# Performance work log

Measured on AMD Instinct MI355X. Metric: run time of the kernel, lower is better.

## Reference

```python
import jax, jax.numpy as jnp
import numpy as np

N, E, P = 50000, 500000, 10000
F_IN, H, C = 128, 256, 1


def gat_conv(x, src, dst, W, a_s, a_d, b):
    # single-head GATConv (PyG): h = x W; e_ij = LeakyReLU(a_s.h_j + a_d.h_i)
    n = x.shape[0]
    h = x @ W                              # [n, out]
    es = h @ a_s                           # [n]
    ed = h @ a_d                           # [n]
    logits = jax.nn.leaky_relu(es[src] + ed[dst], 0.2)   # [E']
    m = jax.ops.segment_max(logits, dst, num_segments=n)
    p = jnp.exp(logits - m[dst])
    denom = jax.ops.segment_sum(p, dst, num_segments=n)
    alpha = p / denom[dst]                 # edge-softmax over incoming edges
    out = jax.ops.segment_sum(h[src] * alpha[:, None], dst, num_segments=n)
    return out + b


def setup_inputs():
    key = jax.random.key(0)
    ks = jax.random.split(key, 14)
    inp = {
        "features": jax.random.normal(ks[0], (N, F_IN), jnp.float32),
        "edge_index": jax.random.randint(ks[1], (2, E), 0, N, dtype=jnp.int32),
        "mask": jax.random.randint(ks[2], (P, 2), 0, N, dtype=jnp.int32),
        "W1": jax.random.normal(ks[3], (F_IN, H), jnp.float32) / np.sqrt(F_IN),
        "a_src1": jax.random.normal(ks[4], (H,), jnp.float32) / np.sqrt(H),
        "a_dst1": jax.random.normal(ks[5], (H,), jnp.float32) / np.sqrt(H),
        "b1": jnp.zeros((H,), jnp.float32),
        "W2": jax.random.normal(ks[6], (H, F_IN), jnp.float32) / np.sqrt(H),
        "a_src2": jax.random.normal(ks[7], (F_IN,), jnp.float32) / np.sqrt(F_IN),
        "a_dst2": jax.random.normal(ks[8], (F_IN,), jnp.float32) / np.sqrt(F_IN),
        "b2": jnp.zeros((F_IN,), jnp.float32),
        "Wl": jax.random.normal(ks[9], (2 * F_IN, C), jnp.float32) / np.sqrt(2 * F_IN),
        "bl": jnp.zeros((C,), jnp.float32),
    }
    return inp


def reference(features, edge_index, mask, W1, a_src1, a_dst1, b1, W2, a_src2, a_dst2, b2, Wl, bl):
    n = features.shape[0]
    loop = jnp.arange(n, dtype=edge_index.dtype)   # PyG add_self_loops=True
    src = jnp.concatenate([edge_index[0], loop])
    dst = jnp.concatenate([edge_index[1], loop])
    h = gat_conv(features, src, dst, W1, a_src1, a_dst1, b1)   # [N, H]
    h = jax.nn.relu(h)                                         # dropout=0.0
    h = gat_conv(h, src, dst, W2, a_src2, a_dst2, b2)          # [N, F_IN]
    mT = mask.T
    p1 = jax.lax.stop_gradient(h[mT[0]])   # .detach() in original
    p2 = jax.lax.stop_gradient(h[mT[1]])
    z = jnp.concatenate([p1, p2], axis=1)  # [P, 2*F_IN]
    return jax.nn.sigmoid(z @ Wl + bl)
```

## Files before the change

### kernel.cpp

```cpp
#include <hip/hip_runtime.h>
#include <hip/hip_bf16.h>
#include <math.h>

#define NN 50000
#define NE 500000
#define NP 10000
#define FIN 128
#define HD 256
#define CAP 64
#define NBG 391

typedef __attribute__((ext_vector_type(8))) short bf16x8;
typedef __attribute__((ext_vector_type(4))) float f32x4;
typedef __attribute__((ext_vector_type(2))) float f32x2;

__device__ inline unsigned short f2bf(float f) {
  unsigned int u = __float_as_uint(f);
  unsigned int r = (u + 0x7fffu + ((u >> 16) & 1u)) >> 16;
  return (unsigned short)r;
}

__device__ inline unsigned int cvtpk_bf16(float lo, float hi) {
  unsigned int r;
  asm("v_cvt_pk_bf16_f32 %0, %1, %2" : "=v"(r) : "v"(lo), "v"(hi));
  return r;
}

__device__ inline float bflo(unsigned int u) { return __uint_as_float(u << 16); }
__device__ inline float bfhi(unsigned int u) { return __uint_as_float(u & 0xffff0000u); }

__device__ inline unsigned char f2fp8(float v) {
  int pk = __builtin_amdgcn_cvt_pk_fp8_f32(v, v, 0, false);
  return (unsigned char)(pk & 0xff);
}

__global__ void init_prep(int* __restrict__ deg,
                          const float* __restrict__ W1, const float* __restrict__ W2,
                          unsigned short* __restrict__ W1T, unsigned short* __restrict__ W2T) {
  int idx = blockIdx.x * 256 + threadIdx.x;
  if (idx < NN) deg[idx] = 0;
  if (idx < FIN * HD) {
    int n = idx / FIN, k = idx - n * FIN;
    W1T[idx] = f2bf(W1[(size_t)k * HD + n]);
    int n2 = idx / HD, k2 = idx - n2 * HD;
    W2T[idx] = f2bf(W2[(size_t)k2 * FIN + n2]);
  }
}

template <int BN, int KTOT, bool A_BF16, bool C_FP8>
__global__ __launch_bounds__(512)
void gemm_hist(const void* __restrict__ Aptr, const unsigned short* __restrict__ BT,
               void* __restrict__ Cptr, const float* __restrict__ a_s,
               const float* __restrict__ a_d, float* __restrict__ es, float* __restrict__ ed,
               int M, const int* __restrict__ dst, int* __restrict__ deg,
               int* __restrict__ rank) {
  if (blockIdx.x >= NBG) {
    int e = (blockIdx.x - NBG) * 512 + threadIdx.x;
    if (e < NE) rank[e] = atomicAdd(&deg[dst[e]], 1);
    return;
  }
  constexpr int LDK = 72;
  constexpr int CN = BN / 2;
  constexpr int NT = CN / 16;
  __shared__ unsigned short As[128][LDK];
  __shared__ unsigned short Bs[BN][LDK];
  __shared__ float esl[128][2];
  __shared__ float edl[128][2];
  const int tid = threadIdx.x;
  const int wave = tid >> 6;
  const int lane = tid & 63;
  const int quad = lane >> 4;
  const int l16 = lane & 15;
  const int wrow = wave >> 1;
  const int wcol = wave & 1;
  const int row0 = blockIdx.x * 128;

  f32x4 acc[2][NT] = {};

  for (int k0 = 0; k0 < KTOT; k0 += 64) {
#pragma unroll
    for (int p = 0; p < 4; p++) {
      int m = p * 32 + (tid >> 4);
      int k4 = (tid & 15) * 4;
      int gr = row0 + m;
      uint2 pk = make_uint2(0u, 0u);
      if (gr < M) {
        if (A_BF16) {
          pk = *(const uint2*)((const unsigned short*)Aptr + (size_t)gr * KTOT + k0 + k4);
        } else {
          float4 v = *(const float4*)((const float*)Aptr + (size_t)gr * KTOT + k0 + k4);
          pk.x = cvtpk_bf16(v.x, v.y);
          pk.y = cvtpk_bf16(v.z, v.w);
        }
      }
      *(uint2*)&As[m][k4] = pk;
    }
#pragma unroll
    for (int p = 0; p < BN / 64; p++) {
      int n = p * 64 + (tid >> 3);
      int k8 = (tid & 7) * 8;
      *(uint4*)&Bs[n][k8] = *(const uint4*)(BT + (size_t)n * KTOT + k0 + k8);
    }
    __syncthreads();
#pragma unroll
    for (int ks = 0; ks < 2; ks++) {
      bf16x8 afrag[2];
#pragma unroll
      for (int rt = 0; rt < 2; rt++)
        afrag[rt] = *(const bf16x8*)&As[wrow * 32 + rt * 16 + l16][ks * 32 + quad * 8];
#pragma unroll
      for (int ct = 0; ct < NT; ct++) {
        bf16x8 bfrag = *(const bf16x8*)&Bs[wcol * CN + ct * 16 + l16][ks * 32 + quad * 8];
#pragma unroll
        for (int rt = 0; rt < 2; rt++)
          acc[rt][ct] = __builtin_amdgcn_mfma_f32_16x16x32_bf16(afrag[rt], bfrag, acc[rt][ct], 0, 0, 0);
      }
    }
    __syncthreads();
  }

  float asv[NT], adv[NT];
#pragma unroll
  for (int ct = 0; ct < NT; ct++) {
    asv[ct] = a_s[wcol * CN + ct * 16 + l16];
    adv[ct] = a_d[wcol * CN + ct * 16 + l16];
  }
#pragma unroll
  for (int rt = 0; rt < 2; rt++) {
#pragma unroll
    for (int r = 0; r < 4; r++) {
      int lrow = wrow * 32 + rt * 16 + quad * 4 + r;
      int grow = row0 + lrow;
      bool ok = (grow < M);
      float ps = 0.f, pd = 0.f;
#pragma unroll
      for (int ct = 0; ct < NT; ct++) {
        float v = acc[rt][ct][r];
        ps += v * asv[ct];
        pd += v * adv[ct];
        if (ok) {
          size_t cidx = (size_t)grow * BN + wcol * CN + ct * 16 + l16;
          if (C_FP8) ((unsigned char*)Cptr)[cidx] = f2fp8(v);
          else       ((unsigned short*)Cptr)[cidx] = f2bf(v);
        }
      }
#pragma unroll
      for (int off = 1; off < 16; off <<= 1) {
        ps += __shfl_xor(ps, off, 16);
        pd += __shfl_xor(pd, off, 16);
      }
      if (l16 == 0) {
        esl[lrow][wcol] = ps;
        edl[lrow][wcol] = pd;
      }
    }
  }
  __syncthreads();
  if (tid < 128) {
    int grow = row0 + tid;
    if (grow < M) {
      es[grow] = esl[tid][0] + esl[tid][1];
      ed[grow] = edl[tid][0] + edl[tid][1];
    }
  }
}

__global__ void scatter_kernel(const int* __restrict__ src, const int* __restrict__ dst,
                               const int* __restrict__ rank, const int* __restrict__ deg,
                               int* __restrict__ ssrc) {
  int t = blockIdx.x * blockDim.x + threadIdx.x;
  int e = t * 2;
  if (e < NE) {
    int2 d2 = *(const int2*)(dst + e);
    int2 s2 = *(const int2*)(src + e);
    int2 r2 = *(const int2*)(rank + e);
    if (r2.x < CAP - 1) ssrc[d2.x * CAP + r2.x] = s2.x;
    if (r2.y < CAP - 1) ssrc[d2.y * CAP + r2.y] = s2.y;
  } else {
    int i = t - NE / 2;
    if (i < NN) ssrc[i * CAP + min(deg[i], CAP - 1)] = i;
  }
}

template <int BN, int KTOT, bool A_BF16, bool C_FP8>
__global__ __launch_bounds__(512)
void mfma_gemm(const void* __restrict__ Aptr, const unsigned short* __restrict__ BT,
               void* __restrict__ Cptr, const float* __restrict__ a_s,
               const float* __restrict__ a_d, float* __restrict__ es, float* __restrict__ ed,
               int M) {
  constexpr int LDK = 72;
  constexpr int CN = BN / 2;
  constexpr int NT = CN / 16;
  __shared__ unsigned short As[128][LDK];
  __shared__ unsigned short Bs[BN][LDK];
  __shared__ float esl[128][2];
  __shared__ float edl[128][2];
  const int tid = threadIdx.x;
  const int wave = tid >> 6;
  const int lane = tid & 63;
  const int quad = lane >> 4;
  const int l16 = lane & 15;
  const int wrow = wave >> 1;
  const int wcol = wave & 1;
  const int row0 = blockIdx.x * 128;

  f32x4 acc[2][NT] = {};

  for (int k0 = 0; k0 < KTOT; k0 += 64) {
#pragma unroll
    for (int p = 0; p < 4; p++) {
      int m = p * 32 + (tid >> 4);
      int k4 = (tid & 15) * 4;
      int gr = row0 + m;
      uint2 pk = make_uint2(0u, 0u);
      if (gr < M) {
        if (A_BF16) {
          pk = *(const uint2*)((const unsigned short*)Aptr + (size_t)gr * KTOT + k0 + k4);
        } else {
          float4 v = *(const float4*)((const float*)Aptr + (size_t)gr * KTOT + k0 + k4);
          pk.x = cvtpk_bf16(v.x, v.y);
          pk.y = cvtpk_bf16(v.z, v.w);
        }
      }
      *(uint2*)&As[m][k4] = pk;
    }
#pragma unroll
    for (int p = 0; p < BN / 64; p++) {
      int n = p * 64 + (tid >> 3);
      int k8 = (tid & 7) * 8;
      *(uint4*)&Bs[n][k8] = *(const uint4*)(BT + (size_t)n * KTOT + k0 + k8);
    }
    __syncthreads();
#pragma unroll
    for (int ks = 0; ks < 2; ks++) {
      bf16x8 afrag[2];
#pragma unroll
      for (int rt = 0; rt < 2; rt++)
        afrag[rt] = *(const bf16x8*)&As[wrow * 32 + rt * 16 + l16][ks * 32 + quad * 8];
#pragma unroll
      for (int ct = 0; ct < NT; ct++) {
        bf16x8 bfrag = *(const bf16x8*)&Bs[wcol * CN + ct * 16 + l16][ks * 32 + quad * 8];
#pragma unroll
        for (int rt = 0; rt < 2; rt++)
          acc[rt][ct] = __builtin_amdgcn_mfma_f32_16x16x32_bf16(afrag[rt], bfrag, acc[rt][ct], 0, 0, 0);
      }
    }
    __syncthreads();
  }

  float asv[NT], adv[NT];
#pragma unroll
  for (int ct = 0; ct < NT; ct++) {
    asv[ct] = a_s[wcol * CN + ct * 16 + l16];
    adv[ct] = a_d[wcol * CN + ct * 16 + l16];
  }
#pragma unroll
  for (int rt = 0; rt < 2; rt++) {
#pragma unroll
    for (int r = 0; r < 4; r++) {
      int lrow = wrow * 32 + rt * 16 + quad * 4 + r;
      int grow = row0 + lrow;
      bool ok = (grow < M);
      float ps = 0.f, pd = 0.f;
#pragma unroll
      for (int ct = 0; ct < NT; ct++) {
        float v = acc[rt][ct][r];
        ps += v * asv[ct];
        pd += v * adv[ct];
        if (ok) {
          size_t cidx = (size_t)grow * BN + wcol * CN + ct * 16 + l16;
          if (C_FP8) ((unsigned char*)Cptr)[cidx] = f2fp8(v);
          else       ((unsigned short*)Cptr)[cidx] = f2bf(v);
        }
      }
#pragma unroll
      for (int off = 1; off < 16; off <<= 1) {
        ps += __shfl_xor(ps, off, 16);
        pd += __shfl_xor(pd, off, 16);
      }
      if (l16 == 0) {
        esl[lrow][wcol] = ps;
        edl[lrow][wcol] = pd;
      }
    }
  }
  __syncthreads();
  if (tid < 128) {
    int grow = row0 + tid;
    if (grow < M) {
      es[grow] = esl[tid][0] + esl[tid][1];
      ed[grow] = edl[tid][0] + edl[tid][1];
    }
  }
}

__global__ __launch_bounds__(256)
void fused_agg64(const int* __restrict__ deg, const int* __restrict__ ssrc,
                 const float* __restrict__ es, const float* __restrict__ ed,
                 const unsigned char* __restrict__ h, const float* __restrict__ bias,
                 unsigned short* __restrict__ outp, int n) {
  int i = blockIdx.x * 16 + (threadIdx.x >> 4);
  int ls = threadIdx.x & 15;
  if (i >= n) return;
  int s = i * CAP;
  int e = s + min(deg[i] + 1, CAP);
  float edv = ed[i];

  float acc[16] = {};
  float lsum = 0.f;
  const unsigned char* hb = h + ls * 16;
  for (int p0 = s; p0 < e; p0 += 16) {
    int p = p0 + ls;
    int msrc = 0;
    float pv = 0.f;
    if (p < e) {
      msrc = ssrc[p];
      float t = es[msrc] + edv;
      float lg = (t > 0.f) ? t : 0.2f * t;
      pv = __expf(lg);
    }
    lsum += pv;
    int cnt = min(16, e - p0);
    int jfull = cnt & ~3;
    for (int j = 0; j < jfull; j += 4) {
      uint4 r[4];
      float w[4];
#pragma unroll
      for (int u = 0; u < 4; u++) {
        int jj = j + u;
        int sj = __shfl(msrc, jj, 16);
        w[u] = __shfl(pv, jj, 16);
        r[u] = *(const uint4*)(hb + (size_t)sj * HD);
      }
#pragma unroll
      for (int u = 0; u < 4; u++) {
        f32x2 lo, hi;
        lo = __builtin_amdgcn_cvt_pk_f32_fp8(r[u].x, false);
        hi = __builtin_amdgcn_cvt_pk_f32_fp8(r[u].x, true);
        acc[0] += w[u] * lo.x; acc[1] += w[u] * lo.y; acc[2] += w[u] * hi.x; acc[3] += w[u] * hi.y;
        lo = __builtin_amdgcn_cvt_pk_f32_fp8(r[u].y, false);
        hi = __builtin_amdgcn_cvt_pk_f32_fp8(r[u].y, true);
        acc[4] += w[u] * lo.x; acc[5] += w[u] * lo.y; acc[6] += w[u] * hi.x; acc[7] += w[u] * hi.y;
        lo = __builtin_amdgcn_cvt_pk_f32_fp8(r[u].z, false);
        hi = __builtin_amdgcn_cvt_pk_f32_fp8(r[u].z, true);
        acc[8] += w[u] * lo.x; acc[9] += w[u] * lo.y; acc[10] += w[u] * hi.x; acc[11] += w[u] * hi.y;
        lo = __builtin_amdgcn_cvt_pk_f32_fp8(r[u].w, false);
        hi = __builtin_amdgcn_cvt_pk_f32_fp8(r[u].w, true);
        acc[12] += w[u] * lo.x; acc[13] += w[u] * lo.y; acc[14] += w[u] * hi.x; acc[15] += w[u] * hi.y;
      }
    }
    if (jfull < cnt) {
      uint4 r[4];
      float w[4];
#pragma unroll
      for (int u = 0; u < 4; u++) {
        int jj = jfull + u;
        bool ok = jj < cnt;
        int jc = ok ? jj : 0;
        int sj = __shfl(msrc, jc, 16);
        float wr = __shfl(pv, jc, 16);
        w[u] = ok ? wr : 0.f;
        r[u] = *(const uint4*)(hb + (size_t)sj * HD);
      }
#pragma unroll
      for (int u = 0; u < 4; u++) {
        f32x2 lo, hi;
        lo = __builtin_amdgcn_cvt_pk_f32_fp8(r[u].x, false);
        hi = __builtin_amdgcn_cvt_pk_f32_fp8(r[u].x, true);
        acc[0] += w[u] * lo.x; acc[1] += w[u] * lo.y; acc[2] += w[u] * hi.x; acc[3] += w[u] * hi.y;
        lo = __builtin_amdgcn_cvt_pk_f32_fp8(r[u].y, false);
        hi = __builtin_amdgcn_cvt_pk_f32_fp8(r[u].y, true);
        acc[4] += w[u] * lo.x; acc[5] += w[u] * lo.y; acc[6] += w[u] * hi.x; acc[7] += w[u] * hi.y;
        lo = __builtin_amdgcn_cvt_pk_f32_fp8(r[u].z, false);
        hi = __builtin_amdgcn_cvt_pk_f32_fp8(r[u].z, true);
        acc[8] += w[u] * lo.x; acc[9] += w[u] * lo.y; acc[10] += w[u] * hi.x; acc[11] += w[u] * hi.y;
        lo = __builtin_amdgcn_cvt_pk_f32_fp8(r[u].w, false);
        hi = __builtin_amdgcn_cvt_pk_f32_fp8(r[u].w, true);
        acc[12] += w[u] * lo.x; acc[13] += w[u] * lo.y; acc[14] += w[u] * hi.x; acc[15] += w[u] * hi.y;
      }
    }
  }
#pragma unroll
  for (int off = 8; off; off >>= 1) lsum += __shfl_xor(lsum, off, 16);
  float invd = 1.0f / lsum;
  float4 b0 = *(const float4*)(bias + ls * 16 + 0);
  float4 b1 = *(const float4*)(bias + ls * 16 + 4);
  float4 b2 = *(const float4*)(bias + ls * 16 + 8);
  float4 b3 = *(const float4*)(bias + ls * 16 + 12);
  float v0 = fmaxf(acc[0] * invd + b0.x, 0.f),  v1 = fmaxf(acc[1] * invd + b0.y, 0.f);
  float v2 = fmaxf(acc[2] * invd + b0.z, 0.f),  v3 = fmaxf(acc[3] * invd + b0.w, 0.f);
  float v4 = fmaxf(acc[4] * invd + b1.x, 0.f),  v5 = fmaxf(acc[5] * invd + b1.y, 0.f);
  float v6 = fmaxf(acc[6] * invd + b1.z, 0.f),  v7 = fmaxf(acc[7] * invd + b1.w, 0.f);
  float v8 = fmaxf(acc[8] * invd + b2.x, 0.f),  v9 = fmaxf(acc[9] * invd + b2.y, 0.f);
  float va = fmaxf(acc[10] * invd + b2.z, 0.f), vb = fmaxf(acc[11] * invd + b2.w, 0.f);
  float vc = fmaxf(acc[12] * invd + b3.x, 0.f), vd = fmaxf(acc[13] * invd + b3.y, 0.f);
  float ve = fmaxf(acc[14] * invd + b3.z, 0.f), vf = fmaxf(acc[15] * invd + b3.w, 0.f);
  unsigned short* ob = outp + (size_t)i * HD + ls * 16;
  *(uint4*)(ob) = make_uint4(cvtpk_bf16(v0, v1), cvtpk_bf16(v2, v3),
                             cvtpk_bf16(v4, v5), cvtpk_bf16(v6, v7));
  *(uint4*)(ob + 8) = make_uint4(cvtpk_bf16(v8, v9), cvtpk_bf16(va, vb),
                                 cvtpk_bf16(vc, vd), cvtpk_bf16(ve, vf));
}

__global__ __launch_bounds__(256)
void fused_agg_l2_pair(const int* __restrict__ deg, const int* __restrict__ ssrc,
                       const float* __restrict__ es, const float* __restrict__ ed,
                       const unsigned short* __restrict__ h, const float* __restrict__ bias,
                       const int* __restrict__ mask, const float* __restrict__ Wl,
                       const float* __restrict__ bl, float* __restrict__ out, int P) {
  constexpr int F = FIN;
  int pair = blockIdx.x * 8 + (threadIdx.x >> 5);
  if (pair >= P) return;
  int l32 = threadIdx.x & 31;
  int hf = l32 >> 4;
  int ls = l32 & 15;
  int i = mask[pair * 2 + hf];
  int s = i * CAP;
  int e = s + min(deg[i] + 1, CAP);
  float edv = ed[i];

  float acc[8] = {};
  float lsum = 0.f;
  const unsigned short* hb = h + ls * 8;
  for (int p0 = s; p0 < e; p0 += 16) {
    int p = p0 + ls;
    int msrc = 0;
    float pv = 0.f;
    if (p < e) {
      msrc = ssrc[p];
      float t = es[msrc] + edv;
      float lg = (t > 0.f) ? t : 0.2f * t;
      pv = __expf(lg);
    }
    lsum += pv;
    int cnt = min(16, e - p0);
    int jfull = cnt & ~3;
    for (int j = 0; j < jfull; j += 4) {
      uint4 r[4];
      float w[4];
#pragma unroll
      for (int u = 0; u < 4; u++) {
        int jj = j + u;
        int sj = __shfl(msrc, jj, 16);
        w[u] = __shfl(pv, jj, 16);
        r[u] = *(const uint4*)(hb + (size_t)sj * F);
      }
#pragma unroll
      for (int u = 0; u < 4; u++) {
        acc[0] += w[u] * bflo(r[u].x); acc[1] += w[u] * bfhi(r[u].x);
        acc[2] += w[u] * bflo(r[u].y); acc[3] += w[u] * bfhi(r[u].y);
        acc[4] += w[u] * bflo(r[u].z); acc[5] += w[u] * bfhi(r[u].z);
        acc[6] += w[u] * bflo(r[u].w); acc[7] += w[u] * bfhi(r[u].w);
      }
    }
    if (jfull < cnt) {
      uint4 r[4];
      float w[4];
#pragma unroll
      for (int u = 0; u < 4; u++) {
        int jj = jfull + u;
        bool ok = jj < cnt;
        int jc = ok ? jj : 0;
        int sj = __shfl(msrc, jc, 16);
        float wr = __shfl(pv, jc, 16);
        w[u] = ok ? wr : 0.f;
        r[u] = *(const uint4*)(hb + (size_t)sj * F);
      }
#pragma unroll
      for (int u = 0; u < 4; u++) {
        acc[0] += w[u] * bflo(r[u].x); acc[1] += w[u] * bfhi(r[u].x);
        acc[2] += w[u] * bflo(r[u].y); acc[3] += w[u] * bfhi(r[u].y);
        acc[4] += w[u] * bflo(r[u].z); acc[5] += w[u] * bfhi(r[u].z);
        acc[6] += w[u] * bflo(r[u].w); acc[7] += w[u] * bfhi(r[u].w);
      }
    }
  }
#pragma unroll
  for (int off = 8; off; off >>= 1) lsum += __shfl_xor(lsum, off, 16);
  float invd = 1.0f / lsum;
  float4 b0 = *(const float4*)(bias + ls * 8 + 0);
  float4 b1 = *(const float4*)(bias + ls * 8 + 4);
  float4 w0 = *(const float4*)(Wl + hf * F + ls * 8 + 0);
  float4 w1 = *(const float4*)(Wl + hf * F + ls * 8 + 4);
  float dotv = (acc[0] * invd + b0.x) * w0.x + (acc[1] * invd + b0.y) * w0.y +
               (acc[2] * invd + b0.z) * w0.z + (acc[3] * invd + b0.w) * w0.w +
               (acc[4] * invd + b1.x) * w1.x + (acc[5] * invd + b1.y) * w1.y +
               (acc[6] * invd + b1.z) * w1.z + (acc[7] * invd + b1.w) * w1.w;
#pragma unroll
  for (int off = 8; off; off >>= 1) dotv += __shfl_xor(dotv, off, 16);
  float othr = __shfl_xor(dotv, 16, 32);
  if (l32 == 0) {
    float z = dotv + othr + bl[0];
    out[pair] = 1.0f / (1.0f + expf(-z));
  }
}

extern "C" void kernel_launch(void* const* d_in, const int* in_sizes, int n_in,
                              void* d_out, int out_size, void* d_ws, size_t ws_size,
                              hipStream_t stream) {
  const float* features = (const float*)d_in[0];
  const int* edge_index = (const int*)d_in[1];
  const int* mask       = (const int*)d_in[2];
  const float* W1     = (const float*)d_in[3];
  const float* a_src1 = (const float*)d_in[4];
  const float* a_dst1 = (const float*)d_in[5];
  const float* b1     = (const float*)d_in[6];
  const float* W2     = (const float*)d_in[7];
  const float* a_src2 = (const float*)d_in[8];
  const float* a_dst2 = (const float*)d_in[9];
  const float* b2     = (const float*)d_in[10];
  const float* Wl     = (const float*)d_in[11];
  const float* bl     = (const float*)d_in[12];
  float* out = (float*)d_out;

  const int* src = edge_index;
  const int* dst = edge_index + NE;

  char* ws = (char*)d_ws;
  size_t off = 0;
  auto alloc = [&](size_t bytes) {
    void* p = ws + off;
    off += (bytes + 255) & ~(size_t)255;
    return p;
  };
  unsigned char* h1q = (unsigned char*)alloc((size_t)NN * HD);
  unsigned short* h2b = (unsigned short*)alloc((size_t)NN * FIN * 2);
  unsigned short* x2b = (unsigned short*)alloc((size_t)NN * HD * 2);
  unsigned short* W1T = (unsigned short*)alloc((size_t)HD * FIN * 2);
  unsigned short* W2T = (unsigned short*)alloc((size_t)FIN * HD * 2);
  float* es_buf  = (float*)alloc((size_t)NN * 4);
  float* ed_buf  = (float*)alloc((size_t)NN * 4);
  int* deg       = (int*)alloc((size_t)NN * 4);
  int* rank      = (int*)alloc((size_t)NE * 4);
  int* ssrc      = (int*)alloc((size_t)NN * CAP * 4);
  (void)ws_size; (void)in_sizes; (void)n_in; (void)out_size;

  const int nblk_n256 = (NN + 255) / 256;
  const int nblk_hist = (NE + 511) / 512;
  const int nblk_scat = (NE / 2 + NN + 255) / 256;

  init_prep<<<nblk_n256, 256, 0, stream>>>(deg, W1, W2, W1T, W2T);
  gemm_hist<HD, FIN, false, true><<<NBG + nblk_hist, 512, 0, stream>>>(
      (const void*)features, W1T, (void*)h1q, a_src1, a_dst1, es_buf, ed_buf, NN,
      dst, deg, rank);
  scatter_kernel<<<nblk_scat, 256, 0, stream>>>(src, dst, rank, deg, ssrc);
  fused_agg64<<<(NN + 15) / 16, 256, 0, stream>>>(
      deg, ssrc, es_buf, ed_buf, h1q, b1, x2b, NN);
  mfma_gemm<FIN, HD, true, false><<<(NN + 127) / 128, 512, 0, stream>>>(
      (const void*)x2b, W2T, (void*)h2b, a_src2, a_dst2, es_buf, ed_buf, NN);
  fused_agg_l2_pair<<<(NP + 7) / 8, 256, 0, stream>>>(
      deg, ssrc, es_buf, ed_buf, h2b, b2, mask, Wl, bl, out, NP);
}
```

Measured before the change: 188.8 us.

## Project layer-2 features onto classifier weights before aggregation

Because the final classifier is linear, the layer-2 GEMM now computes per-node scalar projections h2·Wl[0:128] and h2·Wl[128:256] instead of writing the full bf16 h2 matrix. The pair-prediction kernel then aggregates these scalars with the attention weights rather than gathering 128-wide rows. This removes the h2 write and the wide gather traffic, at the cost of a slightly different floating-point summation order.

```diff
diff --git a/kernel.cpp b/kernel.cpp
--- a/kernel.cpp
+++ b/kernel.cpp
@@ -47,10 +47,10 @@
   }
 }
 
-template <int BN, int KTOT, bool A_BF16, bool C_FP8>
+template <int BN, int KTOT>
 __global__ __launch_bounds__(512)
-void gemm_hist(const void* __restrict__ Aptr, const unsigned short* __restrict__ BT,
-               void* __restrict__ Cptr, const float* __restrict__ a_s,
+void gemm_hist(const float* __restrict__ Aptr, const unsigned short* __restrict__ BT,
+               unsigned char* __restrict__ Cptr, const float* __restrict__ a_s,
                const float* __restrict__ a_d, float* __restrict__ es, float* __restrict__ ed,
                int M, const int* __restrict__ dst, int* __restrict__ deg,
                int* __restrict__ rank) {
@@ -85,13 +85,9 @@
       int gr = row0 + m;
       uint2 pk = make_uint2(0u, 0u);
       if (gr < M) {
-        if (A_BF16) {
-          pk = *(const uint2*)((const unsigned short*)Aptr + (size_t)gr * KTOT + k0 + k4);
-        } else {
-          float4 v = *(const float4*)((const float*)Aptr + (size_t)gr * KTOT + k0 + k4);
-          pk.x = cvtpk_bf16(v.x, v.y);
-          pk.y = cvtpk_bf16(v.z, v.w);
-        }
+        float4 v = *(const float4*)(Aptr + (size_t)gr * KTOT + k0 + k4);
+        pk.x = cvtpk_bf16(v.x, v.y);
+        pk.y = cvtpk_bf16(v.z, v.w);
       }
       *(uint2*)&As[m][k4] = pk;
     }
@@ -140,8 +136,7 @@
         pd += v * adv[ct];
         if (ok) {
           size_t cidx = (size_t)grow * BN + wcol * CN + ct * 16 + l16;
-          if (C_FP8) ((unsigned char*)Cptr)[cidx] = f2fp8(v);
-          else       ((unsigned short*)Cptr)[cidx] = f2bf(v);
+          Cptr[cidx] = f2fp8(v);
         }
       }
 #pragma unroll
@@ -182,12 +177,13 @@
   }
 }
 
-template <int BN, int KTOT, bool A_BF16, bool C_FP8>
+template <int BN, int KTOT>
 __global__ __launch_bounds__(512)
-void mfma_gemm(const void* __restrict__ Aptr, const unsigned short* __restrict__ BT,
-               void* __restrict__ Cptr, const float* __restrict__ a_s,
-               const float* __restrict__ a_d, float* __restrict__ es, float* __restrict__ ed,
-               int M) {
+void gemm2_dots(const unsigned short* __restrict__ Aptr, const unsigned short* __restrict__ BT,
+                const float* __restrict__ a_s, const float* __restrict__ a_d,
+                const float* __restrict__ wl0, const float* __restrict__ wl1,
+                float* __restrict__ es, float* __restrict__ ed,
+                float* __restrict__ g0, float* __restrict__ g1, int M) {
   constexpr int LDK = 72;
   constexpr int CN = BN / 2;
   constexpr int NT = CN / 16;
@@ -195,6 +191,8 @@
   __shared__ unsigned short Bs[BN][LDK];
   __shared__ float esl[128][2];
   __shared__ float edl[128][2];
+  __shared__ float g0l[128][2];
+  __shared__ float g1l[128][2];
   const int tid = threadIdx.x;
   const int wave = tid >> 6;
   const int lane = tid & 63;
@@ -213,15 +211,8 @@
       int k4 = (tid & 15) * 4;
       int gr = row0 + m;
       uint2 pk = make_uint2(0u, 0u);
-      if (gr < M) {
-        if (A_BF16) {
-          pk = *(const uint2*)((const unsigned short*)Aptr + (size_t)gr * KTOT + k0 + k4);
-        } else {
-          float4 v = *(const float4*)((const float*)Aptr + (size_t)gr * KTOT + k0 + k4);
-          pk.x = cvtpk_bf16(v.x, v.y);
-          pk.y = cvtpk_bf16(v.z, v.w);
-        }
-      }
+      if (gr < M)
+        pk = *(const uint2*)(Aptr + (size_t)gr * KTOT + k0 + k4);
       *(uint2*)&As[m][k4] = pk;
     }
 #pragma unroll
@@ -248,39 +239,41 @@
     __syncthreads();
   }
 
-  float asv[NT], adv[NT];
+  float asv[NT], adv[NT], w0v[NT], w1v[NT];
 #pragma unroll
   for (int ct = 0; ct < NT; ct++) {
-    asv[ct] = a_s[wcol * CN + ct * 16 + l16];
-    adv[ct] = a_d[wcol * CN + ct * 16 + l16];
+    int col = wcol * CN + ct * 16 + l16;
+    asv[ct] = a_s[col];
+    adv[ct] = a_d[col];
+    w0v[ct] = wl0[col];
+    w1v[ct] = wl1[col];
   }
 #pragma unroll
   for (int rt = 0; rt < 2; rt++) {
 #pragma unroll
     for (int r = 0; r < 4; r++) {
       int lrow = wrow * 32 + rt * 16 + quad * 4 + r;
-      int grow = row0 + lrow;
-      bool ok = (grow < M);
-      float ps = 0.f, pd = 0.f;
+      float ps = 0.f, pd = 0.f, p0 = 0.f, p1 = 0.f;
 #pragma unroll
       for (int ct = 0; ct < NT; ct++) {
         float v = acc[rt][ct][r];
         ps += v * asv[ct];
         pd += v * adv[ct];
-        if (ok) {
-          size_t cidx = (size_t)grow * BN + wcol * CN + ct * 16 + l16;
-          if (C_FP8) ((unsigned char*)Cptr)[cidx] = f2fp8(v);
-          else       ((unsigned short*)Cptr)[cidx] = f2bf(v);
-        }
+        p0 += v * w0v[ct];
+        p1 += v * w1v[ct];
       }
 #pragma unroll
       for (int off = 1; off < 16; off <<= 1) {
         ps += __shfl_xor(ps, off, 16);
         pd += __shfl_xor(pd, off, 16);
+        p0 += __shfl_xor(p0, off, 16);
+        p1 += __shfl_xor(p1, off, 16);
       }
       if (l16 == 0) {
         esl[lrow][wcol] = ps;
         edl[lrow][wcol] = pd;
+        g0l[lrow][wcol] = p0;
+        g1l[lrow][wcol] = p1;
       }
     }
   }
@@ -290,6 +283,8 @@
     if (grow < M) {
       es[grow] = esl[tid][0] + esl[tid][1];
       ed[grow] = edl[tid][0] + edl[tid][1];
+      g0[grow] = g0l[tid][0] + g0l[tid][1];
+      g1[grow] = g1l[tid][0] + g1l[tid][1];
     }
   }
 }
@@ -403,12 +398,12 @@
 }
 
 __global__ __launch_bounds__(256)
-void fused_agg_l2_pair(const int* __restrict__ deg, const int* __restrict__ ssrc,
-                       const float* __restrict__ es, const float* __restrict__ ed,
-                       const unsigned short* __restrict__ h, const float* __restrict__ bias,
-                       const int* __restrict__ mask, const float* __restrict__ Wl,
-                       const float* __restrict__ bl, float* __restrict__ out, int P) {
-  constexpr int F = FIN;
+void predict_l2(const int* __restrict__ deg, const int* __restrict__ ssrc,
+                const float* __restrict__ es, const float* __restrict__ ed,
+                const float* __restrict__ g0, const float* __restrict__ g1,
+                const float* __restrict__ b2, const int* __restrict__ mask,
+                const float* __restrict__ Wl, const float* __restrict__ bl,
+                float* __restrict__ out, int P) {
   int pair = blockIdx.x * 8 + (threadIdx.x >> 5);
   if (pair >= P) return;
   int l32 = threadIdx.x & 31;
@@ -416,81 +411,34 @@
   int ls = l32 & 15;
   int i = mask[pair * 2 + hf];
   int s = i * CAP;
-  int e = s + min(deg[i] + 1, CAP);
+  int cnt = min(deg[i] + 1, CAP);
   float edv = ed[i];
-
-  float acc[8] = {};
-  float lsum = 0.f;
-  const unsigned short* hb = h + ls * 8;
-  for (int p0 = s; p0 < e; p0 += 16) {
-    int p = p0 + ls;
-    int msrc = 0;
-    float pv = 0.f;
-    if (p < e) {
-      msrc = ssrc[p];
-      float t = es[msrc] + edv;
-      float lg = (t > 0.f) ? t : 0.2f * t;
-      pv = __expf(lg);
-    }
+  const float* g = hf ? g1 : g0;
+
+  float lsum = 0.f, accg = 0.f;
+  for (int k = ls; k < cnt; k += 16) {
+    int m = ssrc[s + k];
+    float t = es[m] + edv;
+    float lg = (t > 0.f) ? t : 0.2f * t;
+    float pv = __expf(lg);
     lsum += pv;
-    int cnt = min(16, e - p0);
-    int jfull = cnt & ~3;
-    for (int j = 0; j < jfull; j += 4) {
-      uint4 r[4];
-      float w[4];
-#pragma unroll
-      for (int u = 0; u < 4; u++) {
-        int jj = j + u;
-        int sj = __shfl(msrc, jj, 16);
-        w[u] = __shfl(pv, jj, 16);
-        r[u] = *(const uint4*)(hb + (size_t)sj * F);
-      }
-#pragma unroll
-      for (int u = 0; u < 4; u++) {
-        acc[0] += w[u] * bflo(r[u].x); acc[1] += w[u] * bfhi(r[u].x);
-        acc[2] += w[u] * bflo(r[u].y); acc[3] += w[u] * bfhi(r[u].y);
-        acc[4] += w[u] * bflo(r[u].z); acc[5] += w[u] * bfhi(r[u].z);
-        acc[6] += w[u] * bflo(r[u].w); acc[7] += w[u] * bfhi(r[u].w);
-      }
-    }
-    if (jfull < cnt) {
-      uint4 r[4];
-      float w[4];
-#pragma unroll
-      for (int u = 0; u < 4; u++) {
-        int jj = jfull + u;
-        bool ok = jj < cnt;
-        int jc = ok ? jj : 0;
-        int sj = __shfl(msrc, jc, 16);
-        float wr = __shfl(pv, jc, 16);
-        w[u] = ok ? wr : 0.f;
-        r[u] = *(const uint4*)(hb + (size_t)sj * F);
-      }
-#pragma unroll
-      for (int u = 0; u < 4; u++) {
-        acc[0] += w[u] * bflo(r[u].x); acc[1] += w[u] * bfhi(r[u].x);
-        acc[2] += w[u] * bflo(r[u].y); acc[3] += w[u] * bfhi(r[u].y);
-        acc[4] += w[u] * bflo(r[u].z); acc[5] += w[u] * bfhi(r[u].z);
-        acc[6] += w[u] * bflo(r[u].w); acc[7] += w[u] * bfhi(r[u].w);
-      }
-    }
-  }
-#pragma unroll
-  for (int off = 8; off; off >>= 1) lsum += __shfl_xor(lsum, off, 16);
-  float invd = 1.0f / lsum;
-  float4 b0 = *(const float4*)(bias + ls * 8 + 0);
-  float4 b1 = *(const float4*)(bias + ls * 8 + 4);
-  float4 w0 = *(const float4*)(Wl + hf * F + ls * 8 + 0);
-  float4 w1 = *(const float4*)(Wl + hf * F + ls * 8 + 4);
-  float dotv = (acc[0] * invd + b0.x) * w0.x + (acc[1] * invd + b0.y) * w0.y +
-               (acc[2] * invd + b0.z) * w0.z + (acc[3] * invd + b0.w) * w0.w +
-               (acc[4] * invd + b1.x) * w1.x + (acc[5] * invd + b1.y) * w1.y +
-               (acc[6] * invd + b1.z) * w1.z + (acc[7] * invd + b1.w) * w1.w;
-#pragma unroll
-  for (int off = 8; off; off >>= 1) dotv += __shfl_xor(dotv, off, 16);
-  float othr = __shfl_xor(dotv, 16, 32);
+    accg += pv * g[m];
+  }
+  float accb = 0.f;
+  const float* wv = Wl + hf * FIN + ls * 8;
+  const float* bv = b2 + ls * 8;
+#pragma unroll
+  for (int q = 0; q < 8; q++) accb += bv[q] * wv[q];
+#pragma unroll
+  for (int off = 8; off; off >>= 1) {
+    lsum += __shfl_xor(lsum, off, 16);
+    accg += __shfl_xor(accg, off, 16);
+    accb += __shfl_xor(accb, off, 16);
+  }
+  float zs = accg / lsum + accb;
+  float othr = __shfl_xor(zs, 16, 32);
   if (l32 == 0) {
-    float z = dotv + othr + bl[0];
+    float z = zs + othr + bl[0];
     out[pair] = 1.0f / (1.0f + expf(-z));
   }
 }
@@ -524,12 +472,13 @@
     return p;
   };
   unsigned char* h1q = (unsigned char*)alloc((size_t)NN * HD);
-  unsigned short* h2b = (unsigned short*)alloc((size_t)NN * FIN * 2);
   unsigned short* x2b = (unsigned short*)alloc((size_t)NN * HD * 2);
   unsigned short* W1T = (unsigned short*)alloc((size_t)HD * FIN * 2);
   unsigned short* W2T = (unsigned short*)alloc((size_t)FIN * HD * 2);
   float* es_buf  = (float*)alloc((size_t)NN * 4);
   float* ed_buf  = (float*)alloc((size_t)NN * 4);
+  float* g0_buf  = (float*)alloc((size_t)NN * 4);
+  float* g1_buf  = (float*)alloc((size_t)NN * 4);
   int* deg       = (int*)alloc((size_t)NN * 4);
   int* rank      = (int*)alloc((size_t)NE * 4);
   int* ssrc      = (int*)alloc((size_t)NN * CAP * 4);
@@ -540,14 +489,13 @@
   const int nblk_scat = (NE / 2 + NN + 255) / 256;
 
   init_prep<<<nblk_n256, 256, 0, stream>>>(deg, W1, W2, W1T, W2T);
-  gemm_hist<HD, FIN, false, true><<<NBG + nblk_hist, 512, 0, stream>>>(
-      (const void*)features, W1T, (void*)h1q, a_src1, a_dst1, es_buf, ed_buf, NN,
-      dst, deg, rank);
+  gemm_hist<HD, FIN><<<NBG + nblk_hist, 512, 0, stream>>>(
+      features, W1T, h1q, a_src1, a_dst1, es_buf, ed_buf, NN, dst, deg, rank);
   scatter_kernel<<<nblk_scat, 256, 0, stream>>>(src, dst, rank, deg, ssrc);
   fused_agg64<<<(NN + 15) / 16, 256, 0, stream>>>(
       deg, ssrc, es_buf, ed_buf, h1q, b1, x2b, NN);
-  mfma_gemm<FIN, HD, true, false><<<(NN + 127) / 128, 512, 0, stream>>>(
-      (const void*)x2b, W2T, (void*)h2b, a_src2, a_dst2, es_buf, ed_buf, NN);
-  fused_agg_l2_pair<<<(NP + 7) / 8, 256, 0, stream>>>(
-      deg, ssrc, es_buf, ed_buf, h2b, b2, mask, Wl, bl, out, NP);
-}
+  gemm2_dots<FIN, HD><<<(NN + 127) / 128, 512, 0, stream>>>(
+      x2b, W2T, a_src2, a_dst2, Wl, Wl + FIN, es_buf, ed_buf, g0_buf, g1_buf, NN);
+  predict_l2<<<(NP + 7) / 8, 256, 0, stream>>>(
+      deg, ssrc, es_buf, ed_buf, g0_buf, g1_buf, b2, mask, Wl, bl, out, NP);
+}
```

Result: faster. 182.8 us (-3.2%).
